# Kernel tuning notes

Measured on AMD Instinct MI355X. Metric: run time of the kernel, lower is better.

The kernel has to match this reference:

```python
import jax, jax.numpy as jnp
import numpy as np

H = 230  # temp_hidden
D = 2 * H  # encoded feature dim = 460


def _lstm(x, Wih, Whh, bih, bhh, reverse=False):
    # x: (B, T, Din) -> (B, T, H); PyTorch gate order i, f, g, o; zero init state
    B = x.shape[0]
    h0 = jnp.zeros((B, H), x.dtype)

    def step(carry, xt):
        h, c = carry
        g = xt @ Wih.T + h @ Whh.T + bih + bhh
        i, f, gg, o = jnp.split(g, 4, axis=-1)
        c = jax.nn.sigmoid(f) * c + jax.nn.sigmoid(i) * jnp.tanh(gg)
        h = jax.nn.sigmoid(o) * jnp.tanh(c)
        return (h, c), h

    _, hs = jax.lax.scan(step, (h0, h0), jnp.swapaxes(x, 0, 1), reverse=reverse)
    return jnp.swapaxes(hs, 0, 1)


def _bilstm(x, Wf, Uf, bf1, bf2, Wb, Ub, bb1, bb2):
    return jnp.concatenate([_lstm(x, Wf, Uf, bf1, bf2),
                            _lstm(x, Wb, Ub, bb1, bb2, reverse=True)], -1)


def _forward(p_features, q_features, score_w, score_b,
             m_Wih_f, m_Whh_f, m_bih_f, m_bhh_f,
             m_Wih_b, m_Whh_b, m_bih_b, m_bhh_b,
             w2a_w, w2a_b, w1a_w, w1a_b,
             b_Wih_f, b_Whh_f, b_bih_f, b_bhh_f,
             b_Wih_b, b_Whh_b, b_bih_b, b_bhh_b):
    # score(cat(p, q, p*q)) decomposed: u[p,q,b] = p.w_p + q.w_q + (p*q).w_pq + bias
    w_p, w_q, w_pq = score_w[0, :D], score_w[0, D:2 * D], score_w[0, 2 * D:]
    u = (jnp.einsum('pbd,d->pb', p_features, w_p)[:, None, :]
         + jnp.einsum('qbd,d->qb', q_features, w_q)[None, :, :]
         + jnp.einsum('pbd,qbd->pqb', p_features * w_pq, q_features)
         + score_b[0])  # (P, Q, B)

    q2c = jnp.transpose(jax.nn.softmax(u, axis=1), (2, 0, 1))  # (B, P, Q)
    c2q = jnp.max(u, axis=1).T                                   # (B, P)

    p_t = jnp.swapaxes(p_features, 0, 1)  # (B, P, D)
    q_t = jnp.swapaxes(q_features, 0, 1)  # (B, Q, D)
    new_u = jnp.einsum('bpq,bqd->bpd', q2c, q_t)  # (B, P, D)
    new_h = c2q[:, :, None] * p_t                  # (B, P, D)

    final_in = jnp.concatenate([p_t, new_h, p_t * new_u, p_t * new_h], -1)  # (B, P, 8H)
    final = _bilstm(final_in, m_Wih_f, m_Whh_f, m_bih_f, m_bhh_f,
                    m_Wih_b, m_Whh_b, m_bih_b, m_bhh_b)  # (B, P, 2H)

    def ptr_scores(h0a):  # h0a: (B, 2H) -> (B, P)
        cat = jnp.concatenate(
            [final, jnp.broadcast_to(h0a[:, None, :], final.shape)], -1)  # (B, P, 4H)
        z = jnp.tanh(jnp.einsum('bpd,ed->bpe', cat, w2a_w) + w2a_b)
        return jnp.einsum('bpe,e->bp', z, w1a_w[0]) + w1a_b[0]

    Bsz = final.shape[0]
    s1 = ptr_scores(jnp.zeros((Bsz, 2 * H), final.dtype))
    alpha1 = jax.nn.softmax(s1, axis=1)                       # (B, P)
    c1 = jnp.einsum('bp,bpd->bd', alpha1, final)[:, None, :]  # (B, 1, 2H)
    h0a = _bilstm(c1, b_Wih_f, b_Whh_f, b_bih_f, b_bhh_f,
                  b_Wih_b, b_Whh_b, b_bih_b, b_bhh_b)[:, 0, :]  # (B, 2H)
    alpha2 = jax.nn.log_softmax(ptr_scores(h0a), axis=1)
    return final, jnp.log(alpha1), alpha2


def setup_inputs() -> dict:
    key = jax.random.key(0)
    ks = jax.random.split(key, 24)
    P, Q, B = 512, 64, 32
    s = 0.05

    def rn(k, shape):
        return jax.random.normal(k, shape, jnp.float32) * s

    return {
        'p_features': jax.random.normal(ks[0], (P, B, D), jnp.float32),
        'q_features': jax.random.normal(ks[1], (Q, B, D), jnp.float32),
        'score_w': rn(ks[2], (1, 3 * D)), 'score_b': rn(ks[3], (1,)),
        'm_Wih_f': rn(ks[4], (4 * H, 8 * H)), 'm_Whh_f': rn(ks[5], (4 * H, H)),
        'm_bih_f': rn(ks[6], (4 * H,)), 'm_bhh_f': rn(ks[7], (4 * H,)),
        'm_Wih_b': rn(ks[8], (4 * H, 8 * H)), 'm_Whh_b': rn(ks[9], (4 * H, H)),
        'm_bih_b': rn(ks[10], (4 * H,)), 'm_bhh_b': rn(ks[11], (4 * H,)),
        'w2a_w': rn(ks[12], (2 * H, 4 * H)), 'w2a_b': rn(ks[13], (2 * H,)),
        'w1a_w': rn(ks[14], (1, 2 * H)), 'w1a_b': rn(ks[15], (1,)),
        'b_Wih_f': rn(ks[16], (4 * H, 2 * H)), 'b_Whh_f': rn(ks[17], (4 * H, H)),
        'b_bih_f': rn(ks[18], (4 * H,)), 'b_bhh_f': rn(ks[19], (4 * H,)),
        'b_Wih_b': rn(ks[20], (4 * H, 2 * H)), 'b_Whh_b': rn(ks[21], (4 * H, H)),
        'b_bih_b': rn(ks[22], (4 * H,)), 'b_bhh_b': rn(ks[23], (4 * H,)),
    }


def reference(p_features, q_features, score_w, score_b,
              m_Wih_f, m_Whh_f, m_bih_f, m_bhh_f,
              m_Wih_b, m_Whh_b, m_bih_b, m_bhh_b,
              w2a_w, w2a_b, w1a_w, w1a_b,
              b_Wih_f, b_Whh_f, b_bih_f, b_bhh_f,
              b_Wih_b, b_Whh_b, b_bih_b, b_bhh_b):
    return _forward(p_features, q_features, score_w, score_b,
                    m_Wih_f, m_Whh_f, m_bih_f, m_bhh_f,
                    m_Wih_b, m_Whh_b, m_bih_b, m_bhh_b,
                    w2a_w, w2a_b, w1a_w, w1a_b,
                    b_Wih_f, b_Whh_f, b_bih_f, b_bhh_f,
                    b_Wih_b, b_Whh_b, b_bih_b, b_bhh_b)
```

## Files before the change

kernel.cpp:

```cpp
#include <hip/hip_runtime.h>

#define HH 230
#define DD 460
#define PPn 512
#define QQn 64
#define BBn 32
#define G4 920
#define K1 1840
#define KP1 1856
#define MRn 16384
#define KP3 480
#define LDFB 480

typedef _Float16 f16;
typedef f16 half2v __attribute__((ext_vector_type(2)));
typedef short bf16x8_t __attribute__((ext_vector_type(8)));
typedef float f32x4_t __attribute__((ext_vector_type(4)));

__device__ __forceinline__ float sigm(float x) { return 1.0f / (1.0f + __expf(-x)); }
__device__ __forceinline__ float tanhfast(float x) { return 1.0f - 2.0f / (__expf(2.0f * x) + 1.0f); }

__device__ __forceinline__ unsigned short f2bf(float x) {
  unsigned int u = __builtin_bit_cast(unsigned int, x);
  unsigned int r = (u + 0x7fffu + ((u >> 16) & 1u)) >> 16;
  return (unsigned short)r;
}
__device__ __forceinline__ float bf2f(unsigned short h) {
  unsigned int u = ((unsigned int)h) << 16;
  return __builtin_bit_cast(float, u);
}

__device__ __forceinline__ float dot2f(half2v a, half2v b, float c) {
#if __has_builtin(__builtin_amdgcn_fdot2)
  return __builtin_amdgcn_fdot2(a, b, c, false);
#else
  return c + (float)a.x * (float)b.x + (float)a.y * (float)b.y;
#endif
}

static constexpr size_t SZ_X   = (size_t)MRn * G4 * 4;
static constexpr size_t OFF_XF = 0;
static constexpr size_t OFF_XB = OFF_XF + SZ_X;
static constexpr size_t OFF_FI = OFF_XB + SZ_X;
static constexpr size_t SZ_FI  = (size_t)MRn * KP1 * 2;
static constexpr size_t OFF_Y  = OFF_FI;
static constexpr size_t OFF_FB = OFF_FI + (size_t)MRn * DD * 4;
static constexpr size_t OFF_WFP = OFF_FI + SZ_FI;
static constexpr size_t SZ_WP1  = (size_t)1024 * KP1 * 2;
static constexpr size_t OFF_WBP = OFF_WFP + SZ_WP1;
static constexpr size_t OFF_W2P = OFF_WBP + SZ_WP1;
static constexpr size_t SZ_W2P  = (size_t)512 * KP3 * 2;
static constexpr size_t OFF_WPF = OFF_W2P + SZ_W2P;
static constexpr size_t SZ_WPK  = (size_t)115 * G4 * 4;
static constexpr size_t OFF_WPB = ((OFF_WPF + SZ_WPK + 255) & ~(size_t)255);
static constexpr size_t OFF_WTF = ((OFF_WPB + SZ_WPK + 255) & ~(size_t)255);
static constexpr size_t SZ_WT   = (size_t)DD * G4 * 4;
static constexpr size_t OFF_WTB = OFF_WTF + SZ_WT;
static constexpr size_t OFF_BIASF = OFF_WTB + SZ_WT;
static constexpr size_t OFF_BIASB = ((OFF_BIASF + G4 * 4 + 255) & ~(size_t)255);
static constexpr size_t OFF_SP  = ((OFF_BIASB + G4 * 4 + 255) & ~(size_t)255);
static constexpr size_t OFF_SQ  = OFF_SP + (size_t)PPn * BBn * 4;
static constexpr size_t OFF_S1  = OFF_SQ + (size_t)QQn * BBn * 4;
static constexpr size_t OFF_AL1 = OFF_S1 + (size_t)MRn * 4;
static constexpr size_t OFF_C1  = OFF_AL1 + (size_t)MRn * 4;
static constexpr size_t OFF_H0A = ((OFF_C1 + (size_t)BBn * DD * 4 + 255) & ~(size_t)255);
static constexpr size_t OFF_HR  = ((OFF_H0A + (size_t)BBn * DD * 4 + 255) & ~(size_t)255);
static constexpr size_t OFF_S2  = ((OFF_HR + (size_t)BBn * DD * 4 + 255) & ~(size_t)255);

__global__ __launch_bounds__(256) void k_pad_wih(const float* __restrict__ Wf, const float* __restrict__ Wb,
                                                 unsigned short* __restrict__ Pf, unsigned short* __restrict__ Pb) {
  size_t idx = (size_t)blockIdx.x * 256 + threadIdx.x;
  int n = (int)(idx / KP1), k = (int)(idx % KP1);
  const float* W = blockIdx.y ? Wb : Wf;
  unsigned short* Pp = blockIdx.y ? Pb : Pf;
  float v = (n < G4 && k < K1) ? W[(size_t)n * K1 + k] : 0.f;
  Pp[idx] = f2bf(v);
}

__global__ __launch_bounds__(256) void k_pad_w2a(const float* __restrict__ W, unsigned short* __restrict__ Pq) {
  size_t idx = (size_t)blockIdx.x * 256 + threadIdx.x;
  int n = (int)(idx / KP3), k = (int)(idx % KP3);
  float v = (n < DD && k < DD) ? W[(size_t)n * G4 + k] : 0.f;
  Pq[idx] = f2bf(v);
}

__global__ __launch_bounds__(256) void k_pack_whh(const float* __restrict__ Wf, const float* __restrict__ Wb,
                                                  unsigned int* __restrict__ Pf, unsigned int* __restrict__ Pb) {
  int idx = blockIdx.x * 256 + threadIdx.x;
  if (idx >= 115 * G4) return;
  int kk = idx / G4, row = idx % G4;
  const float* W = blockIdx.y ? Wb : Wf;
  unsigned int* Pp = blockIdx.y ? Pb : Pf;
  half2v h; h.x = (f16)W[(size_t)row * HH + 2 * kk]; h.y = (f16)W[(size_t)row * HH + 2 * kk + 1];
  Pp[idx] = __builtin_bit_cast(unsigned int, h);
}

__global__ __launch_bounds__(256) void k_pack_bwih(const float* __restrict__ Wf, const float* __restrict__ Wb,
                                                   float* __restrict__ Tf, float* __restrict__ Tb) {
  int idx = blockIdx.x * 256 + threadIdx.x;
  if (idx >= DD * G4) return;
  int d = idx / G4, row = idx % G4;
  const float* W = blockIdx.y ? Wb : Wf;
  float* T = blockIdx.y ? Tb : Tf;
  T[idx] = W[(size_t)row * DD + d];
}

__global__ __launch_bounds__(256) void k_bias(const float* __restrict__ bihF, const float* __restrict__ bhhF,
                                              const float* __restrict__ bihB, const float* __restrict__ bhhB,
                                              float* __restrict__ biasF, float* __restrict__ biasB) {
  int i = blockIdx.x * 256 + threadIdx.x;
  if (i < G4) {
    if (blockIdx.y == 0) biasF[i] = bihF[i] + bhhF[i];
    else biasB[i] = bihB[i] + bhhB[i];
  }
}

__global__ __launch_bounds__(256) void k_fbpad(unsigned short* __restrict__ FB) {
  int i = blockIdx.x * 256 + threadIdx.x;
  int r = i / 20, j = i % 20;
  FB[(size_t)r * LDFB + DD + j] = 0;
}

__global__ __launch_bounds__(256) void k_rowdot(const float* __restrict__ M, const float* __restrict__ w,
                                                float* __restrict__ out) {
  int r = blockIdx.x * 4 + (threadIdx.x >> 6);
  int lane = threadIdx.x & 63;
  const float* row = M + (size_t)r * DD;
  float acc = 0.f;
  for (int d = lane; d < DD; d += 64) acc += row[d] * w[d];
#pragma unroll
  for (int d = 1; d < 64; d <<= 1) acc += __shfl_xor(acc, d, 64);
  if (lane == 0) out[r] = acc;
}

__global__ __launch_bounds__(256) void k_attn(const float* __restrict__ p_feat, const float* __restrict__ q_feat,
                                              const float* __restrict__ score_w, const float* __restrict__ score_b,
                                              const float* __restrict__ sp, const float* __restrict__ sq,
                                              unsigned short* __restrict__ FIp) {
  __shared__ half2v q_s[64 * 230];
  __shared__ half2v p_s[32 * 230];
  __shared__ half2v wpq[230];
  __shared__ float sq_s[64];
  __shared__ float u_row[64];
  __shared__ __align__(16) float w_row[64];
  __shared__ float mxs[1];

  int tid = threadIdx.x;
  int b = blockIdx.y;
  int p0 = blockIdx.x * 32;

  for (int i = tid; i < 230; i += 256) {
    half2v w; w.x = (f16)score_w[2 * DD + 2 * i]; w.y = (f16)score_w[2 * DD + 2 * i + 1];
    wpq[i] = w;
  }
  for (int i = tid; i < 64; i += 256) sq_s[i] = sq[i * BBn + b];
  for (int q = 0; q < 64; q++) {
    for (int i = tid; i < 230; i += 256) {
      float2 f2 = *(const float2*)(q_feat + ((size_t)(q * BBn + b)) * DD + 2 * i);
      half2v v; v.x = (f16)f2.x; v.y = (f16)f2.y;
      q_s[q * 230 + i] = v;
    }
  }
  for (int pl = 0; pl < 32; pl++) {
    for (int i = tid; i < 230; i += 256) {
      float2 f2 = *(const float2*)(p_feat + ((size_t)((p0 + pl) * BBn + b)) * DD + 2 * i);
      half2v v; v.x = (f16)f2.x; v.y = (f16)f2.y;
      p_s[pl * 230 + i] = v;
    }
  }
  __syncthreads();

  float sbias = score_b[0];
  int lane = tid & 63, wv = tid >> 6;
  int myq = tid >> 2, quarter = tid & 3;
  int kb = quarter * 58;
  int ke = (kb + 58 < 230) ? (kb + 58) : 230;

  for (int pl = 0; pl < 32; pl++) {
    float acc = 0.f;
    const half2v* prow = p_s + pl * 230;
    const half2v* qrow = q_s + myq * 230;
    for (int k = kb; k < ke; k++) {
      half2v pw = prow[k] * wpq[k];
      acc = dot2f(pw, qrow[k], acc);
    }
    acc += __shfl_xor(acc, 1, 64);
    acc += __shfl_xor(acc, 2, 64);
    if (quarter == 0) u_row[myq] = acc + sp[(p0 + pl) * BBn + b] + sq_s[myq] + sbias;
    __syncthreads();
    if (wv == 0) {
      float v = u_row[lane];
      float m = v;
#pragma unroll
      for (int d = 1; d < 64; d <<= 1) m = fmaxf(m, __shfl_xor(m, d, 64));
      float e = __expf(v - m);
      float s = e;
#pragma unroll
      for (int d = 1; d < 64; d <<= 1) s += __shfl_xor(s, d, 64);
      w_row[lane] = e / s;
      if (lane == 0) mxs[0] = m;
    }
    __syncthreads();
    if (tid < 230) {
      float c2q = mxs[0];
      half2v pv = p_s[pl * 230 + tid];
      float nux = 0.f, nuy = 0.f;
      for (int q = 0; q < 64; q += 4) {
        float4 wq = *(const float4*)&w_row[q];
        half2v q0 = q_s[(q + 0) * 230 + tid];
        half2v q1 = q_s[(q + 1) * 230 + tid];
        half2v q2 = q_s[(q + 2) * 230 + tid];
        half2v q3 = q_s[(q + 3) * 230 + tid];
        nux = fmaf(wq.x, (float)q0.x, nux); nuy = fmaf(wq.x, (float)q0.y, nuy);
        nux = fmaf(wq.y, (float)q1.x, nux); nuy = fmaf(wq.y, (float)q1.y, nuy);
        nux = fmaf(wq.z, (float)q2.x, nux); nuy = fmaf(wq.z, (float)q2.y, nuy);
        nux = fmaf(wq.w, (float)q3.x, nux); nuy = fmaf(wq.w, (float)q3.y, nuy);
      }
      float px = (float)pv.x, py = (float)pv.y;
      size_t rr = (size_t)(b * PPn + p0 + pl);
      unsigned short* o = FIp + rr * KP1 + 2 * tid;
      *(unsigned int*)(o +    0) = (unsigned int)f2bf(px)            | ((unsigned int)f2bf(py) << 16);
      *(unsigned int*)(o +  460) = (unsigned int)f2bf(c2q * px)      | ((unsigned int)f2bf(c2q * py) << 16);
      *(unsigned int*)(o +  920) = (unsigned int)f2bf(px * nux)      | ((unsigned int)f2bf(py * nuy) << 16);
      *(unsigned int*)(o + 1380) = (unsigned int)f2bf(c2q * px * px) | ((unsigned int)f2bf(c2q * py * py) << 16);
    } else if (tid < 238) {
      int j = tid - 230;
      size_t rr = (size_t)(b * PPn + p0 + pl);
      *(unsigned int*)(FIp + rr * KP1 + 1840 + 2 * j) = 0u;
    }
    __syncthreads();
  }
}

__global__ __launch_bounds__(256, 2) void k_gemm(const unsigned short* __restrict__ A, int lda,
                                                 const unsigned short* __restrict__ Bw, int ldb,
                                                 float* __restrict__ C, int ldc,
                                                 int Nreal, int Ktiles, const float* __restrict__ bias) {
  __shared__ unsigned short As[128 * 32];
  __shared__ unsigned short Bs[128 * 32];
  int tid = threadIdx.x;
  int m0 = blockIdx.x * 128, n0 = blockIdx.y * 128;
  int wv = tid >> 6, lane = tid & 63;
  int wr = wv >> 1, wc = wv & 1;
  int laneM = lane & 15, laneK = lane >> 4;

  f32x4_t acc[4][4];
#pragma unroll
  for (int i = 0; i < 4; i++)
#pragma unroll
    for (int j = 0; j < 4; j++) acc[i][j] = (f32x4_t){0.f, 0.f, 0.f, 0.f};

  int row0 = tid >> 2, ch0 = tid & 3;
  int row1 = (256 + tid) >> 2, ch1 = tid & 3;
  const unsigned short* a0 = A + (size_t)(m0 + row0) * lda + ch0 * 8;
  const unsigned short* a1 = A + (size_t)(m0 + row1) * lda + ch1 * 8;
  const unsigned short* b0 = Bw + (size_t)(n0 + row0) * ldb + ch0 * 8;
  const unsigned short* b1 = Bw + (size_t)(n0 + row1) * ldb + ch1 * 8;

  for (int kt = 0; kt < Ktiles; kt++) {
    uint4 av0 = *(const uint4*)a0;
    uint4 av1 = *(const uint4*)a1;
    uint4 bv0 = *(const uint4*)b0;
    uint4 bv1 = *(const uint4*)b1;
    a0 += 32; a1 += 32; b0 += 32; b1 += 32;
    __syncthreads();
    *(uint4*)(As + (size_t)tid * 8)         = av0;
    *(uint4*)(As + (size_t)(256 + tid) * 8) = av1;
    *(uint4*)(Bs + (size_t)tid * 8)         = bv0;
    *(uint4*)(Bs + (size_t)(256 + tid) * 8) = bv1;
    __syncthreads();
    bf16x8_t af[4], bfr[4];
#pragma unroll
    for (int mi = 0; mi < 4; mi++)
      af[mi] = *(const bf16x8_t*)(As + (size_t)(wr * 64 + mi * 16 + laneM) * 32 + laneK * 8);
#pragma unroll
    for (int ni = 0; ni < 4; ni++)
      bfr[ni] = *(const bf16x8_t*)(Bs + (size_t)(wc * 64 + ni * 16 + laneM) * 32 + laneK * 8);
#pragma unroll
    for (int mi = 0; mi < 4; mi++)
#pragma unroll
      for (int ni = 0; ni < 4; ni++)
        acc[mi][ni] = __builtin_amdgcn_mfma_f32_16x16x32_bf16(af[mi], bfr[ni], acc[mi][ni], 0, 0, 0);
  }
#pragma unroll
  for (int mi = 0; mi < 4; mi++)
#pragma unroll
    for (int ni = 0; ni < 4; ni++) {
      int ccol = n0 + wc * 64 + ni * 16 + laneM;
      if (ccol < Nreal) {
        float bv = bias ? bias[ccol] : 0.f;
#pragma unroll
        for (int j = 0; j < 4; j++) {
          int crow = m0 + wr * 64 + mi * 16 + laneK * 4 + j;
          C[(size_t)crow * ldc + ccol] = acc[mi][ni][j] + bv;
        }
      }
    }
}

__global__ __launch_bounds__(512, 2) void k_recur(const unsigned int* __restrict__ WPf,
                                                  const unsigned int* __restrict__ WPb,
                                                  const float* __restrict__ Xf, const float* __restrict__ Xb,
                                                  float* __restrict__ outF, unsigned short* __restrict__ FB) {
  __shared__ unsigned int h2[2][116];
  __shared__ float abuf[232];
  int tid = threadIdx.x;
  int dir = blockIdx.x >> 5, b = blockIdx.x & 31;
  const unsigned int* WP = dir ? WPb : WPf;
  const float* X = dir ? Xb : Xf;

  bool isA = tid < 230;
  bool isB = (tid >= 256) && (tid < 486);
  bool act = isA || isB;
  int u = isA ? tid : (tid - 256);
  int row0 = isA ? u : (HH + u);
  int row1 = isA ? (2 * HH + u) : (3 * HH + u);

  half2v w0[115], w1[115];
  if (act) {
#pragma unroll
    for (int k = 0; k < 115; k++) {
      w0[k] = __builtin_bit_cast(half2v, WP[k * G4 + row0]);
      w1[k] = __builtin_bit_cast(half2v, WP[k * G4 + row1]);
    }
  }
  for (int i = tid; i < 116; i += 512) { h2[0][i] = 0u; h2[1][i] = 0u; }

  int col0 = u + (isB ? HH : 0);
  int col1 = col0 + 2 * HH;
  float x0 = 0.f, x1 = 0.f;
  if (act) {
    int t0 = dir ? (PPn - 1) : 0;
    const float* xr = X + (size_t)(b * PPn + t0) * G4;
    x0 = xr[col0]; x1 = xr[col1];
  }
  float c = 0.f;
  __syncthreads();

  for (int s = 0; s < PPn; s++) {
    int t = dir ? (PPn - 1 - s) : s;
    float acc0 = x0, acc1 = x1;
    if (act && s < PPn - 1) {
      int tn = dir ? (PPn - 2 - s) : (s + 1);
      const float* xr = X + (size_t)(b * PPn + tn) * G4;
      x0 = xr[col0]; x1 = xr[col1];
    }
    const unsigned int* hb = h2[s & 1];
    if (act) {
#pragma unroll
      for (int ch = 0; ch < 28; ch++) {
        uint4 hv = *(const uint4*)(hb + ch * 4);
        half2v ha = __builtin_bit_cast(half2v, hv.x);
        half2v hbv = __builtin_bit_cast(half2v, hv.y);
        half2v hc = __builtin_bit_cast(half2v, hv.z);
        half2v hd = __builtin_bit_cast(half2v, hv.w);
        acc0 = dot2f(w0[ch * 4 + 0], ha, acc0);  acc1 = dot2f(w1[ch * 4 + 0], ha, acc1);
        acc0 = dot2f(w0[ch * 4 + 1], hbv, acc0); acc1 = dot2f(w1[ch * 4 + 1], hbv, acc1);
        acc0 = dot2f(w0[ch * 4 + 2], hc, acc0);  acc1 = dot2f(w1[ch * 4 + 2], hc, acc1);
        acc0 = dot2f(w0[ch * 4 + 3], hd, acc0);  acc1 = dot2f(w1[ch * 4 + 3], hd, acc1);
      }
      uint2 hv2 = *(const uint2*)(hb + 112);
      half2v ha = __builtin_bit_cast(half2v, hv2.x);
      half2v hbv = __builtin_bit_cast(half2v, hv2.y);
      acc0 = dot2f(w0[112], ha, acc0);  acc1 = dot2f(w1[112], ha, acc1);
      acc0 = dot2f(w0[113], hbv, acc0); acc1 = dot2f(w1[113], hbv, acc1);
      half2v hc = __builtin_bit_cast(half2v, hb[114]);
      acc0 = dot2f(w0[114], hc, acc0);  acc1 = dot2f(w1[114], hc, acc1);
    }
    float ff = 0.f, oo = 0.f;
    if (isA) {
      abuf[u] = sigm(acc0) * tanhfast(acc1);
    }
    if (isB) { ff = sigm(acc0); oo = sigm(acc1); }
    __syncthreads();
    if (isB) {
      c = ff * c + abuf[u];
      float hval = oo * tanhfast(c);
      f16* hw = (f16*)(&h2[(s + 1) & 1][0]);
      hw[u] = (f16)hval;
      size_t ro = (size_t)(b * PPn + t);
      outF[ro * DD + dir * HH + u] = hval;
      FB[ro * LDFB + dir * HH + u] = f2bf(hval);
    }
    __syncthreads();
  }
}

__global__ __launch_bounds__(256) void k_score(const float* __restrict__ Yv, const float* __restrict__ hR,
                                               const float* __restrict__ w1a, const float* __restrict__ w1b,
                                               float* __restrict__ out) {
  int r = blockIdx.x * 4 + (threadIdx.x >> 6);
  int lane = threadIdx.x & 63;
  const float* row = Yv + (size_t)r * DD;
  const float* hrow = hR ? (hR + (size_t)(r >> 9) * DD) : nullptr;
  float acc = 0.f;
  for (int e = lane; e < DD; e += 64) {
    float v = row[e];
    if (hrow) v += hrow[e];
    acc += tanhfast(v) * w1a[e];
  }
#pragma unroll
  for (int d = 1; d < 64; d <<= 1) acc += __shfl_xor(acc, d, 64);
  if (lane == 0) out[r] = acc + w1b[0];
}

__global__ __launch_bounds__(512) void k_softmax(const float* __restrict__ s, float* __restrict__ outLog,
                                                 float* __restrict__ outAlpha) {
  __shared__ float red[8];
  int b = blockIdx.x, t = threadIdx.x;
  int lane = t & 63, wv = t >> 6;
  float v = s[b * PPn + t];
  float m = v;
#pragma unroll
  for (int d = 1; d < 64; d <<= 1) m = fmaxf(m, __shfl_xor(m, d, 64));
  if (lane == 0) red[wv] = m;
  __syncthreads();
  float mall = red[0];
#pragma unroll
  for (int i = 1; i < 8; i++) mall = fmaxf(mall, red[i]);
  __syncthreads();
  float e = __expf(v - mall);
  float sum = e;
#pragma unroll
  for (int d = 1; d < 64; d <<= 1) sum += __shfl_xor(sum, d, 64);
  if (lane == 0) red[wv] = sum;
  __syncthreads();
  float tot = red[0];
#pragma unroll
  for (int i = 1; i < 8; i++) tot += red[i];
  float lz = __logf(tot);
  outLog[b * PPn + t] = v - mall - lz;
  if (outAlpha) outAlpha[b * PPn + t] = e / tot;
}

__global__ __launch_bounds__(256) void k_c1(const float* __restrict__ alpha1, const float* __restrict__ finalF,
                                            float* __restrict__ c1) {
  __shared__ float al[512];
  int b = blockIdx.x, t = threadIdx.x;
  al[t] = alpha1[b * PPn + t];
  al[t + 256] = alpha1[b * PPn + t + 256];
  __syncthreads();
  for (int d = t; d < DD; d += 256) {
    float acc = 0.f;
#pragma unroll 8
    for (int p = 0; p < PPn; p++) acc += al[p] * finalF[((size_t)b * PPn + p) * DD + d];
    c1[b * DD + d] = acc;
  }
}

__global__ __launch_bounds__(256) void k_h0a(const float* __restrict__ WTf, const float* __restrict__ WTb,
                                             const float* __restrict__ bihF, const float* __restrict__ bhhF,
                                             const float* __restrict__ bihB, const float* __restrict__ bhhB,
                                             const float* __restrict__ c1, float* __restrict__ h0a) {
  int dir = blockIdx.x >> 5, b = blockIdx.x & 31;
  const float* WT = dir ? WTb : WTf;
  const float* bih = dir ? bihB : bihF;
  const float* bhh = dir ? bhhB : bhhF;
  __shared__ float cs[DD];
  int t = threadIdx.x;
  for (int d = t; d < DD; d += 256) cs[d] = c1[b * DD + d];
  __syncthreads();
  if (t < HH) {
    float gi = bih[t] + bhh[t];
    float gg = bih[2 * HH + t] + bhh[2 * HH + t];
    float go = bih[3 * HH + t] + bhh[3 * HH + t];
    for (int d = 0; d < DD; d++) {
      float cv = cs[d];
      const float* wr2 = WT + (size_t)d * G4;
      gi = fmaf(cv, wr2[t], gi);
      gg = fmaf(cv, wr2[2 * HH + t], gg);
      go = fmaf(cv, wr2[3 * HH + t], go);
    }
    float cc = sigm(gi) * tanhfast(gg);
    h0a[b * DD + dir * HH + t] = sigm(go) * tanhfast(cc);
  }
}

__global__ __launch_bounds__(256) void k_hR(const float* __restrict__ w2a_w, const float* __restrict__ h0a,
                                            float* __restrict__ hR) {
  int b = blockIdx.x, t = threadIdx.x;
  __shared__ float hs[DD];
  for (int d = t; d < DD; d += 256) hs[d] = h0a[b * DD + d];
  __syncthreads();
  for (int e = t; e < DD; e += 256) {
    float acc = 0.f;
    const float* wr2 = w2a_w + (size_t)e * G4 + DD;
    for (int d = 0; d < DD; d++) acc = fmaf(hs[d], wr2[d], acc);
    hR[b * DD + e] = acc;
  }
}

extern "C" void kernel_launch(void* const* d_in, const int* in_sizes, int n_in,
                              void* d_out, int out_size, void* d_ws, size_t ws_size,
                              hipStream_t stream) {
  (void)in_sizes; (void)n_in; (void)out_size; (void)ws_size;
  const float* p_feat  = (const float*)d_in[0];
  const float* q_feat  = (const float*)d_in[1];
  const float* score_w = (const float*)d_in[2];
  const float* score_b = (const float*)d_in[3];
  const float* mWihF   = (const float*)d_in[4];
  const float* mWhhF   = (const float*)d_in[5];
  const float* mBihF   = (const float*)d_in[6];
  const float* mBhhF   = (const float*)d_in[7];
  const float* mWihB   = (const float*)d_in[8];
  const float* mWhhB   = (const float*)d_in[9];
  const float* mBihB   = (const float*)d_in[10];
  const float* mBhhB   = (const float*)d_in[11];
  const float* w2a_w   = (const float*)d_in[12];
  const float* w2a_b   = (const float*)d_in[13];
  const float* w1a_w   = (const float*)d_in[14];
  const float* w1a_b   = (const float*)d_in[15];
  const float* bWihF   = (const float*)d_in[16];
  const float* bBihF   = (const float*)d_in[18];
  const float* bBhhF   = (const float*)d_in[19];
  const float* bWihB   = (const float*)d_in[20];
  const float* bBihB   = (const float*)d_in[22];
  const float* bBhhB   = (const float*)d_in[23];

  char* ws = (char*)d_ws;
  float* XF = (float*)(ws + OFF_XF);
  float* XB = (float*)(ws + OFF_XB);
  unsigned short* FI = (unsigned short*)(ws + OFF_FI);
  float* Yv = (float*)(ws + OFF_Y);
  unsigned short* FB = (unsigned short*)(ws + OFF_FB);
  unsigned short* WFP = (unsigned short*)(ws + OFF_WFP);
  unsigned short* WBP = (unsigned short*)(ws + OFF_WBP);
  unsigned short* W2P = (unsigned short*)(ws + OFF_W2P);
  unsigned int* WPF = (unsigned int*)(ws + OFF_WPF);
  unsigned int* WPB = (unsigned int*)(ws + OFF_WPB);
  float* WTF = (float*)(ws + OFF_WTF);
  float* WTB = (float*)(ws + OFF_WTB);
  float* BIASF = (float*)(ws + OFF_BIASF);
  float* BIASB = (float*)(ws + OFF_BIASB);
  float* SP = (float*)(ws + OFF_SP);
  float* SQ = (float*)(ws + OFF_SQ);
  float* S1 = (float*)(ws + OFF_S1);
  float* AL1 = (float*)(ws + OFF_AL1);
  float* C1 = (float*)(ws + OFF_C1);
  float* H0A = (float*)(ws + OFF_H0A);
  float* HR = (float*)(ws + OFF_HR);
  float* S2 = (float*)(ws + OFF_S2);

  float* outF = (float*)d_out;
  float* outLA1 = outF + (size_t)BBn * PPn * DD;
  float* outA2 = outLA1 + (size_t)BBn * PPn;

  k_pad_wih<<<dim3(7424, 2), 256, 0, stream>>>(mWihF, mWihB, WFP, WBP);
  k_pad_w2a<<<dim3(960), 256, 0, stream>>>(w2a_w, W2P);
  k_pack_whh<<<dim3(414, 2), 256, 0, stream>>>(mWhhF, mWhhB, WPF, WPB);
  k_pack_bwih<<<dim3(1654, 2), 256, 0, stream>>>(bWihF, bWihB, WTF, WTB);
  k_bias<<<dim3(4, 2), 256, 0, stream>>>(mBihF, mBhhF, mBihB, mBhhB, BIASF, BIASB);
  k_fbpad<<<dim3(1280), 256, 0, stream>>>(FB);
  k_rowdot<<<dim3(4096), 256, 0, stream>>>(p_feat, score_w, SP);
  k_rowdot<<<dim3(512), 256, 0, stream>>>(q_feat, score_w + DD, SQ);
  k_attn<<<dim3(16, 32), 256, 0, stream>>>(p_feat, q_feat, score_w, score_b, SP, SQ, FI);
  k_gemm<<<dim3(128, 8), 256, 0, stream>>>(FI, KP1, WFP, KP1, XF, G4, G4, 58, BIASF);
  k_gemm<<<dim3(128, 8), 256, 0, stream>>>(FI, KP1, WBP, KP1, XB, G4, G4, 58, BIASB);
  k_recur<<<dim3(64), 512, 0, stream>>>(WPF, WPB, XF, XB, outF, FB);
  k_gemm<<<dim3(128, 4), 256, 0, stream>>>(FB, KP3, W2P, KP3, Yv, DD, DD, 15, w2a_b);
  k_score<<<dim3(4096), 256, 0, stream>>>(Yv, nullptr, w1a_w, w1a_b, S1);
  k_softmax<<<dim3(32), 512, 0, stream>>>(S1, outLA1, AL1);
  k_c1<<<dim3(32), 256, 0, stream>>>(AL1, outF, C1);
  k_h0a<<<dim3(64), 256, 0, stream>>>(WTF, WTB, bBihF, bBhhF, bBihB, bBhhB, C1, H0A);
  k_hR<<<dim3(32), 256, 0, stream>>>(w2a_w, H0A, HR);
  k_score<<<dim3(4096), 256, 0, stream>>>(Yv, HR, w1a_w, w1a_b, S2);
  k_softmax<<<dim3(32), 512, 0, stream>>>(S2, outA2, nullptr);
}
```

Baseline: 1.652 ms.

## Assign one gate row per thread in LSTM recurrence, spill weight tail to LDS

The recurrent kernel now launches 960 threads per block with one gate row per thread, replacing 512 threads that each handled two rows. This halves the serial dot-product chain per thread each timestep, which is the latency-critical path of the 512-step scan. Each thread keeps 104 packed weight pairs in registers and puts the remaining 11 in LDS to stay within the register budget at this block size. The cost is extra LDS reads per step and a wider block that must synchronise twice per step.

```diff
diff --git a/kernel.cpp b/kernel.cpp
--- a/kernel.cpp
+++ b/kernel.cpp
@@ -37,6 +37,7 @@
   return c + (float)a.x * (float)b.x + (float)a.y * (float)b.y;
 #endif
 }
+__device__ __forceinline__ half2v bch2(unsigned int u) { return __builtin_bit_cast(half2v, u); }
 
 static constexpr size_t SZ_X   = (size_t)MRn * G4 * 4;
 static constexpr size_t OFF_XF = 0;
@@ -298,84 +299,75 @@
     }
 }
 
-__global__ __launch_bounds__(512, 2) void k_recur(const unsigned int* __restrict__ WPf,
-                                                  const unsigned int* __restrict__ WPb,
-                                                  const float* __restrict__ Xf, const float* __restrict__ Xb,
-                                                  float* __restrict__ outF, unsigned short* __restrict__ FB) {
+__global__ __launch_bounds__(960, 1)
+void k_recur(const unsigned int* __restrict__ WPf,
+             const unsigned int* __restrict__ WPb,
+             const float* __restrict__ Xf, const float* __restrict__ Xb,
+             float* __restrict__ outF, unsigned short* __restrict__ FB) {
+  __shared__ unsigned int wlds[920 * 12];
   __shared__ unsigned int h2[2][116];
-  __shared__ float abuf[232];
+  __shared__ float gbuf[3][232];
   int tid = threadIdx.x;
   int dir = blockIdx.x >> 5, b = blockIdx.x & 31;
-  const unsigned int* WP = dir ? WPb : WPf;
-  const float* X = dir ? Xb : Xf;
-
-  bool isA = tid < 230;
-  bool isB = (tid >= 256) && (tid < 486);
-  bool act = isA || isB;
-  int u = isA ? tid : (tid - 256);
-  int row0 = isA ? u : (HH + u);
-  int row1 = isA ? (2 * HH + u) : (3 * HH + u);
-
-  half2v w0[115], w1[115];
+  const unsigned int* __restrict__ WP = dir ? WPb : WPf;
+  const float* __restrict__ X = dir ? Xb : Xf;
+
+  bool act = tid < 920;
+  int row = tid;
+  int gate = row / 230;
+  int u = row - gate * 230;
+
+  half2v w[104];
   if (act) {
 #pragma unroll
-    for (int k = 0; k < 115; k++) {
-      w0[k] = __builtin_bit_cast(half2v, WP[k * G4 + row0]);
-      w1[k] = __builtin_bit_cast(half2v, WP[k * G4 + row1]);
-    }
-  }
-  for (int i = tid; i < 116; i += 512) { h2[0][i] = 0u; h2[1][i] = 0u; }
-
-  int col0 = u + (isB ? HH : 0);
-  int col1 = col0 + 2 * HH;
-  float x0 = 0.f, x1 = 0.f;
-  if (act) {
-    int t0 = dir ? (PPn - 1) : 0;
-    const float* xr = X + (size_t)(b * PPn + t0) * G4;
-    x0 = xr[col0]; x1 = xr[col1];
-  }
+    for (int k = 0; k < 104; k++) w[k] = bch2(WP[k * G4 + row]);
+    unsigned int* sl = &wlds[row * 12];
+#pragma unroll
+    for (int j = 0; j < 11; j++) sl[j] = WP[(104 + j) * G4 + row];
+    sl[11] = 0u;
+  }
+  for (int i = tid; i < 116; i += 960) { h2[0][i] = 0u; h2[1][i] = 0u; }
+
+  float x0 = 0.f;
+  if (act) x0 = X[(size_t)(b * PPn + (dir ? PPn - 1 : 0)) * G4 + row];
   float c = 0.f;
   __syncthreads();
 
   for (int s = 0; s < PPn; s++) {
     int t = dir ? (PPn - 1 - s) : s;
-    float acc0 = x0, acc1 = x1;
+    float acc = x0;
     if (act && s < PPn - 1) {
       int tn = dir ? (PPn - 2 - s) : (s + 1);
-      const float* xr = X + (size_t)(b * PPn + tn) * G4;
-      x0 = xr[col0]; x1 = xr[col1];
+      x0 = X[(size_t)(b * PPn + tn) * G4 + row];
     }
     const unsigned int* hb = h2[s & 1];
     if (act) {
 #pragma unroll
-      for (int ch = 0; ch < 28; ch++) {
+      for (int ch = 0; ch < 26; ch++) {
         uint4 hv = *(const uint4*)(hb + ch * 4);
-        half2v ha = __builtin_bit_cast(half2v, hv.x);
-        half2v hbv = __builtin_bit_cast(half2v, hv.y);
-        half2v hc = __builtin_bit_cast(half2v, hv.z);
-        half2v hd = __builtin_bit_cast(half2v, hv.w);
-        acc0 = dot2f(w0[ch * 4 + 0], ha, acc0);  acc1 = dot2f(w1[ch * 4 + 0], ha, acc1);
-        acc0 = dot2f(w0[ch * 4 + 1], hbv, acc0); acc1 = dot2f(w1[ch * 4 + 1], hbv, acc1);
-        acc0 = dot2f(w0[ch * 4 + 2], hc, acc0);  acc1 = dot2f(w1[ch * 4 + 2], hc, acc1);
-        acc0 = dot2f(w0[ch * 4 + 3], hd, acc0);  acc1 = dot2f(w1[ch * 4 + 3], hd, acc1);
+        acc = dot2f(w[ch * 4 + 0], bch2(hv.x), acc);
+        acc = dot2f(w[ch * 4 + 1], bch2(hv.y), acc);
+        acc = dot2f(w[ch * 4 + 2], bch2(hv.z), acc);
+        acc = dot2f(w[ch * 4 + 3], bch2(hv.w), acc);
       }
-      uint2 hv2 = *(const uint2*)(hb + 112);
-      half2v ha = __builtin_bit_cast(half2v, hv2.x);
-      half2v hbv = __builtin_bit_cast(half2v, hv2.y);
-      acc0 = dot2f(w0[112], ha, acc0);  acc1 = dot2f(w1[112], ha, acc1);
-      acc0 = dot2f(w0[113], hbv, acc0); acc1 = dot2f(w1[113], hbv, acc1);
-      half2v hc = __builtin_bit_cast(half2v, hb[114]);
-      acc0 = dot2f(w0[114], hc, acc0);  acc1 = dot2f(w1[114], hc, acc1);
-    }
-    float ff = 0.f, oo = 0.f;
-    if (isA) {
-      abuf[u] = sigm(acc0) * tanhfast(acc1);
-    }
-    if (isB) { ff = sigm(acc0); oo = sigm(acc1); }
-    __syncthreads();
-    if (isB) {
-      c = ff * c + abuf[u];
-      float hval = oo * tanhfast(c);
+      const unsigned int* sl = &wlds[row * 12];
+#pragma unroll
+      for (int j = 0; j < 3; j++) {
+        uint4 wv = *(const uint4*)(sl + 4 * j);
+        uint4 hv = *(const uint4*)(hb + 104 + 4 * j);
+        acc = dot2f(bch2(wv.x), bch2(hv.x), acc);
+        acc = dot2f(bch2(wv.y), bch2(hv.y), acc);
+        acc = dot2f(bch2(wv.z), bch2(hv.z), acc);
+        acc = dot2f(bch2(wv.w), bch2(hv.w), acc);
+      }
+      if (gate == 0)      gbuf[0][u] = sigm(acc);
+      else if (gate == 1) gbuf[1][u] = sigm(acc);
+      else if (gate == 2) gbuf[2][u] = tanhfast(acc);
+    }
+    __syncthreads();
+    if (act && gate == 3) {
+      c = gbuf[1][u] * c + gbuf[0][u] * gbuf[2][u];
+      float hval = sigm(acc) * tanhfast(c);
       f16* hw = (f16*)(&h2[(s + 1) & 1][0]);
       hw[u] = (f16)hval;
       size_t ro = (size_t)(b * PPn + t);
@@ -556,7 +548,7 @@
   k_attn<<<dim3(16, 32), 256, 0, stream>>>(p_feat, q_feat, score_w, score_b, SP, SQ, FI);
   k_gemm<<<dim3(128, 8), 256, 0, stream>>>(FI, KP1, WFP, KP1, XF, G4, G4, 58, BIASF);
   k_gemm<<<dim3(128, 8), 256, 0, stream>>>(FI, KP1, WBP, KP1, XB, G4, G4, 58, BIASB);
-  k_recur<<<dim3(64), 512, 0, stream>>>(WPF, WPB, XF, XB, outF, FB);
+  k_recur<<<dim3(64), 960, 0, stream>>>(WPF, WPB, XF, XB, outF, FB);
   k_gemm<<<dim3(128, 4), 256, 0, stream>>>(FB, KP3, W2P, KP3, Yv, DD, DD, 15, w2a_b);
   k_score<<<dim3(4096), 256, 0, stream>>>(Yv, nullptr, w1a_w, w1a_b, S1);
   k_softmax<<<dim3(32), 512, 0, stream>>>(S1, outLA1, AL1);
```

After: 1.602 ms. -3.1%, faster.
